# Kernel tuning notes

Measured on AMD Instinct MI355X. Metric: run time of the kernel, lower is better.

## Reference

```python
import jax, jax.numpy as jnp
import numpy as np

DIM = 1024
HEADS = 16
HEAD_DIM = DIM // HEADS
SCALE = DIM ** -0.5  # note: original uses full dim, not head_dim


def setup_inputs() -> dict:
    key = jax.random.key(0)
    k1, k2, k3, k4 = jax.random.split(key, 4)
    x = jax.random.normal(k1, (4, 2048, DIM), dtype=jnp.float32)
    # nn.Linear(dim, 3*dim, bias=False): weight [3*dim, dim]; y = x @ W.T
    w_qkv = jax.random.normal(k2, (3 * DIM, DIM), dtype=jnp.float32) * (DIM ** -0.5)
    w_out = jax.random.normal(k3, (DIM, DIM), dtype=jnp.float32) * (DIM ** -0.5)
    b_out = jax.random.normal(k4, (DIM,), dtype=jnp.float32) * 0.01
    return {"x": x, "w_qkv": w_qkv, "w_out": w_out, "b_out": b_out}


def reference(x, w_qkv, w_out, b_out):
    b, n, d = x.shape
    qkv = jnp.einsum('bnd,ed->bne', x, w_qkv)  # [b, n, 3*dim]
    # rearrange 'b n (qkv h d) -> qkv b h n d'
    qkv = qkv.reshape(b, n, 3, HEADS, HEAD_DIM).transpose(2, 0, 3, 1, 4)
    q, k, v = qkv[0], qkv[1], qkv[2]
    dots = jnp.einsum('bhid,bhjd->bhij', q, k) * SCALE
    attn = jax.nn.softmax(dots, axis=-1)
    out = jnp.einsum('bhij,bhjd->bhid', attn, v)
    out = out.transpose(0, 2, 1, 3).reshape(b, n, d)  # b h n d -> b n (h d)
    return jnp.einsum('bnd,ed->bne', out, w_out) + b_out
```

## Files before the change

kernel.cpp:

```cpp
#include <hip/hip_runtime.h>
#include <stdint.h>
#include <stddef.h>

typedef _Float16 f16;
typedef __attribute__((ext_vector_type(8))) _Float16 f16x8;
typedef __attribute__((ext_vector_type(4))) _Float16 f16x4;
typedef __attribute__((ext_vector_type(4))) float f32x4;

#define DINL __device__ __forceinline__

DINL void async_cp16(void* lds, const void* gmem) {
    __builtin_amdgcn_global_load_lds(
        (const __attribute__((address_space(1))) void*)(uintptr_t)gmem,
        (__attribute__((address_space(3))) void*)(uint32_t)(uintptr_t)lds,
        16, 0, 0);
}

__global__ void cast_fused(const float* __restrict__ x, f16* __restrict__ xh,
                           const float* __restrict__ wq, f16* __restrict__ wqh,
                           const float* __restrict__ wo, f16* __restrict__ woh,
                           float qs) {
    int stride = gridDim.x * blockDim.x;
    for (int i = blockIdx.x * blockDim.x + threadIdx.x; i < 3145728; i += stride) {
        const float4* src; f16x4* dst; float s = 1.f;
        if (i < 2097152)      { src = (const float4*)x  + i;            dst = (f16x4*)xh  + i; }
        else if (i < 2883584) { int j = i - 2097152; src = (const float4*)wq + j; dst = (f16x4*)wqh + j;
                                if (j < 262144) s = qs; }
        else                  { int j = i - 2883584; src = (const float4*)wo + j; dst = (f16x4*)woh + j; }
        float4 v = *src;
        f16x4 h = { (f16)(v.x * s), (f16)(v.y * s), (f16)(v.z * s), (f16)(v.w * s) };
        *dst = h;
    }
}

template <typename TC, bool HAS_BIAS>
__global__ __launch_bounds__(512, 2) void gemm8p(
    const f16* __restrict__ A, const f16* __restrict__ B,
    TC* __restrict__ C, const float* __restrict__ bias,
    int M, int N, int K)
{
    __shared__ __align__(16) char lds[98304];

    const int tid  = threadIdx.x;
    const int lane = tid & 63;
    const int wave = tid >> 6;
    const int rlo  = lane & 15;
    const int hi   = lane >> 4;
    const int wm   = wave & 3;
    const int wn   = wave >> 2;
    const int bm   = blockIdx.y * 256;
    const int bn   = blockIdx.x * 128;

    const int rA = tid >> 2;
    const int lc = (tid & 3) ^ ((tid >> 3) & 3);
    const f16* pA0 = A + (size_t)(bm + rA) * K + lc * 8;
    const f16* pA1 = A + (size_t)(bm + 128 + rA) * K + lc * 8;
    const f16* pB  = B + (size_t)(bn + rA) * K + lc * 8;
    const uint32_t dst0 = (uint32_t)tid * 16;
    const uint32_t dst1 = 8192u + (uint32_t)tid * 16;
    const uint32_t dstB = (uint32_t)tid * 16;

    const int fsw = (rlo >> 1) & 3;
    uint32_t afb[4], bfb[4];
#pragma unroll
    for (int m = 0; m < 4; ++m)
        afb[m] = (uint32_t)(wm * 64 + m * 16 + rlo) * 64 + (uint32_t)((hi ^ fsw) << 4);
#pragma unroll
    for (int n = 0; n < 4; ++n)
        bfb[n] = (uint32_t)(wn * 64 + n * 16 + rlo) * 64 + (uint32_t)((hi ^ fsw) << 4);

    f32x4 acc[4][4] = {};
    const int NP = K >> 5;

    auto stage = [&](int sg) {
        const uint32_t sa = (uint32_t)(sg & 3) << 14;
        const uint32_t sb = 65536u + ((uint32_t)(sg & 3) << 13);
        async_cp16(lds + sa + dst0, pA0);
        async_cp16(lds + sa + dst1, pA1);
        async_cp16(lds + sb + dstB, pB);
        pA0 += 32; pA1 += 32; pB += 32;
    };

    stage(0); stage(1); stage(2);

    for (int g = 0; g < NP; ++g) {
        if (g + 2 < NP)      asm volatile("s_waitcnt vmcnt(6)" ::: "memory");
        else if (g + 1 < NP) asm volatile("s_waitcnt vmcnt(3)" ::: "memory");
        else                 asm volatile("s_waitcnt vmcnt(0)" ::: "memory");
        __builtin_amdgcn_s_barrier();
        asm volatile("" ::: "memory");
        __builtin_amdgcn_sched_barrier(0);

        if (g + 3 < NP) stage(g + 3);

        const uint32_t sa = (uint32_t)(g & 3) << 14;
        const uint32_t sb = 65536u + ((uint32_t)(g & 3) << 13);

        f16x8 af[4], bf[4];
#pragma unroll
        for (int m = 0; m < 4; ++m)
            af[m] = *(const f16x8*)(lds + sa + afb[m]);
#pragma unroll
        for (int n = 0; n < 4; ++n)
            bf[n] = *(const f16x8*)(lds + sb + bfb[n]);

        __builtin_amdgcn_s_setprio(1);
#pragma unroll
        for (int m = 0; m < 4; ++m)
#pragma unroll
            for (int n = 0; n < 4; ++n)
                acc[m][n] = __builtin_amdgcn_mfma_f32_16x16x32_f16(af[m], bf[n], acc[m][n], 0, 0, 0);
        __builtin_amdgcn_s_setprio(0);
    }

#pragma unroll
    for (int n = 0; n < 4; ++n) {
        const int gc = bn + wn * 64 + n * 16 + rlo;
        float bv = 0.f;
        if constexpr (HAS_BIAS) bv = bias[gc];
#pragma unroll
        for (int m = 0; m < 4; ++m) {
            const int gr0 = bm + wm * 64 + m * 16 + (hi << 2);
#pragma unroll
            for (int r = 0; r < 4; ++r) {
                float v = acc[m][n][r] + bv;
                if constexpr (sizeof(TC) == 4) C[(size_t)(gr0 + r) * N + gc] = v;
                else                           C[(size_t)(gr0 + r) * N + gc] = (f16)v;
            }
        }
    }
}

__global__ __launch_bounds__(256) void transpose_v(const f16* __restrict__ qkv, f16* __restrict__ vt) {
    __shared__ float T[64][65];
    const int bid = blockIdx.x, bh = bid >> 5, st = bid & 31;
    const int b = bh >> 4, h = bh & 15, s0 = st * 64;
    const int tid = threadIdx.x;
    const int rs = tid >> 2, c0 = (tid & 3) * 16;
    const f16* src = &qkv[(size_t)(b * 2048 + s0 + rs) * 3072 + 2048 + h * 64 + c0];
    f16x8 v0 = ((const f16x8*)src)[0], v1 = ((const f16x8*)src)[1];
#pragma unroll
    for (int e = 0; e < 8; ++e) { T[rs][c0 + e] = (float)v0[e]; T[rs][c0 + 8 + e] = (float)v1[e]; }
    __syncthreads();
    const int rd = tid >> 2, k0 = (tid & 3) * 16;
    f16x8 w0, w1;
#pragma unroll
    for (int e = 0; e < 8; ++e) { w0[e] = (f16)T[k0 + e][rd]; w1[e] = (f16)T[k0 + 8 + e][rd]; }
    f16* dst = &vt[(size_t)(bh * 64 + rd) * 2048 + s0 + k0];
    ((f16x8*)dst)[0] = w0; ((f16x8*)dst)[1] = w1;
}

DINL int phi_row(int r) {
    return (r & 32) | ((r & 12) << 1) | ((r & 16) >> 2) | (r & 3);
}

__global__ __launch_bounds__(256, 4) void attn_mfma(
    const f16* __restrict__ qkv, const f16* __restrict__ vt, f16* __restrict__ out)
{
    constexpr int TD = 3072;
    constexpr int KSTR = 64 * TD;
    __shared__ __align__(16) f16 Ks[2][64 * 64];
    __shared__ __align__(16) f16 Vs[2][64 * 64];

    const int tid = threadIdx.x, lane = tid & 63, wave = tid >> 6;
    const int bh = blockIdx.x, b = bh >> 4, h = bh & 15;
    const int q0 = blockIdx.y * 128;
    const size_t base = (size_t)b * 2048 * TD + h * 64;
    const int lo = lane & 15, hi = lane >> 4;

    f16x8 qf[2][2];
#pragma unroll
    for (int g = 0; g < 2; ++g) {
        const f16* qp = &qkv[base + (size_t)(q0 + wave * 32 + g * 16 + lo) * TD + hi * 8];
        qf[g][0] = *(const f16x8*)qp;
        qf[g][1] = *(const f16x8*)(qp + 32);
    }

    const int s1 = tid,        r1 = s1 >> 3, c1 = (s1 & 7) ^ (r1 & 7);
    const int s2 = tid + 256,  r2 = s2 >> 3, c2 = (s2 & 7) ^ (r2 & 7);
    const f16* kg1 = &qkv[base + 1024 + (size_t)phi_row(r1) * TD + c1 * 8];
    const f16* kg2 = &qkv[base + 1024 + (size_t)phi_row(r2) * TD + c2 * 8];
    const f16* vg1 = &vt[(size_t)(bh * 64 + r1) * 2048 + c1 * 8];
    const f16* vg2 = &vt[(size_t)(bh * 64 + r2) * 2048 + c2 * 8];
    f16* kd1 = &Ks[0][s1 * 8]; f16* kd2 = &Ks[0][s2 * 8];
    f16* vd1 = &Vs[0][s1 * 8]; f16* vd2 = &Vs[0][s2 * 8];

    async_cp16(kd1, kg1); async_cp16(kd2, kg2);
    async_cp16(vd1, vg1); async_cp16(vd2, vg2);
    kg1 += KSTR; kg2 += KSTR; vg1 += 64; vg2 += 64;

    float lsum[2] = {};
    f32x4 o_[2][4] = {};

    for (int jt = 0; jt < 32; ++jt) {
        const int cur = jt & 1;
        __syncthreads();
        if (jt + 1 < 32) {
            const int nb = (cur ^ 1) * 4096;
            async_cp16(kd1 + nb, kg1); async_cp16(kd2 + nb, kg2);
            async_cp16(vd1 + nb, vg1); async_cp16(vd2 + nb, vg2);
            kg1 += KSTR; kg2 += KSTR; vg1 += 64; vg2 += 64;
        }

        f32x4 sc[2][4] = {{}, {}};
        __builtin_amdgcn_s_setprio(1);
#pragma unroll
        for (int ks = 0; ks < 2; ++ks) {
            const int c = ks * 4 + hi;
#pragma unroll
            for (int n = 0; n < 4; ++n) {
                int kr = n * 16 + lo;
                f16x8 kf = *(const f16x8*)&Ks[cur][(kr * 8 + (c ^ (kr & 7))) * 8];
                sc[0][n] = __builtin_amdgcn_mfma_f32_16x16x32_f16(kf, qf[0][ks], sc[0][n], 0, 0, 0);
                sc[1][n] = __builtin_amdgcn_mfma_f32_16x16x32_f16(kf, qf[1][ks], sc[1][n], 0, 0, 0);
            }
        }
        __builtin_amdgcn_s_setprio(0);

        f16x8 pa[2][2];
#pragma unroll
        for (int g = 0; g < 2; ++g)
#pragma unroll
        for (int n = 0; n < 4; ++n) {
            float p0 = exp2f(sc[g][n][0]), p1 = exp2f(sc[g][n][1]);
            float p2 = exp2f(sc[g][n][2]), p3 = exp2f(sc[g][n][3]);
            lsum[g] += (p0 + p1) + (p2 + p3);
            const int off = (n & 1) * 4;
            const int w = n >> 1;
            pa[g][w][off]   = (f16)p0; pa[g][w][off+1] = (f16)p1;
            pa[g][w][off+2] = (f16)p2; pa[g][w][off+3] = (f16)p3;
        }

        __builtin_amdgcn_s_setprio(1);
#pragma unroll
        for (int ks = 0; ks < 2; ++ks) {
            const int c = ks * 4 + hi;
#pragma unroll
            for (int n = 0; n < 4; ++n) {
                int dd = n * 16 + lo;
                f16x8 vb = *(const f16x8*)&Vs[cur][(dd * 8 + (c ^ (dd & 7))) * 8];
                o_[0][n] = __builtin_amdgcn_mfma_f32_16x16x32_f16(pa[0][ks], vb, o_[0][n], 0, 0, 0);
                o_[1][n] = __builtin_amdgcn_mfma_f32_16x16x32_f16(pa[1][ks], vb, o_[1][n], 0, 0, 0);
            }
        }
        __builtin_amdgcn_s_setprio(0);
    }

#pragma unroll
    for (int g = 0; g < 2; ++g) {
        float ls = lsum[g];
        ls += __shfl_xor(ls, 16);
        ls += __shfl_xor(ls, 32);
#pragma unroll
        for (int r = 0; r < 4; ++r) {
            float inv = 1.f / __shfl(ls, hi * 4 + r);
            int row = q0 + wave * 32 + g * 16 + hi * 4 + r;
#pragma unroll
            for (int n = 0; n < 4; ++n) {
                int dim = h * 64 + n * 16 + lo;
                out[(size_t)(b * 2048 + row) * 1024 + dim] = (f16)(o_[g][n][r] * inv);
            }
        }
    }
}

extern "C" void kernel_launch(void* const* d_in, const int* in_sizes, int n_in,
                              void* d_out, int out_size, void* d_ws, size_t ws_size,
                              hipStream_t stream)
{
    int ix = 0, iq = 1, iw = 2, ib = 3;
    for (int i = 0; i < n_in; ++i) {
        if      (in_sizes[i] == 8388608) ix = i;
        else if (in_sizes[i] == 3145728) iq = i;
        else if (in_sizes[i] == 1048576) iw = i;
        else if (in_sizes[i] == 1024)    ib = i;
    }
    const float* x     = (const float*)d_in[ix];
    const float* w_qkv = (const float*)d_in[iq];
    const float* w_out = (const float*)d_in[iw];
    const float* b_out = (const float*)d_in[ib];

    char* ws = (char*)d_ws;
    f16* Xh    = (f16*)(ws + 0);
    f16* AOh   = Xh;
    f16* Wqkvh = (f16*)(ws + 16777216);
    f16* QKVh  = (f16*)(ws + 23068672);
    f16* Vth   = (f16*)(ws + 73400320);
    f16* Wouth = (f16*)(ws + 90177536);

    const float QSCALE = 0.03125f * 1.4426950408889634f;

    cast_fused<<<3072, 256, 0, stream>>>(x, Xh, w_qkv, Wqkvh, w_out, Wouth, QSCALE);

    gemm8p<f16, false><<<dim3(24, 32), 512, 0, stream>>>(
        Xh, Wqkvh, QKVh, nullptr, 8192, 3072, 1024);

    transpose_v<<<2048, 256, 0, stream>>>(QKVh, Vth);

    attn_mfma<<<dim3(64, 16), 256, 0, stream>>>(QKVh, Vth, AOh);

    gemm8p<float, true><<<dim3(8, 32), 512, 0, stream>>>(
        AOh, Wouth, (float*)d_out, b_out, 8192, 1024, 1024);
}
```

Measured before the change: 290.1 us.

## Software-pipeline PV MFMA one tile behind QK with triple-buffered V

Restructures the attention loop so that the P·V matmul for the previous key tile runs after the current tile's QK^T MFMAs and before its exp2 softmax. The intent is to overlap exp/convert VALU work with MFMA work. V is now triple-buffered in LDS so the previous tile's V stays valid while the next one is being prefetched. Probabilities are also packed with cvt_pkrtz into f16 pairs instead of scalar casts. The cost is more LDS use per block, which may reduce occupancy, and higher register pressure from keeping pa live across iterations.

```diff
diff --git a/kernel.cpp b/kernel.cpp
--- a/kernel.cpp
+++ b/kernel.cpp
@@ -5,9 +5,14 @@
 typedef _Float16 f16;
 typedef __attribute__((ext_vector_type(8))) _Float16 f16x8;
 typedef __attribute__((ext_vector_type(4))) _Float16 f16x4;
+typedef __attribute__((ext_vector_type(2))) _Float16 f16x2;
 typedef __attribute__((ext_vector_type(4))) float f32x4;
 
 #define DINL __device__ __forceinline__
+
+DINL f16x2 pkrtz(float a, float b) {
+    return __builtin_bit_cast(f16x2, __builtin_amdgcn_cvt_pkrtz(a, b));
+}
 
 DINL void async_cp16(void* lds, const void* gmem) {
     __builtin_amdgcn_global_load_lds(
@@ -159,8 +164,8 @@
 {
     constexpr int TD = 3072;
     constexpr int KSTR = 64 * TD;
-    __shared__ __align__(16) f16 Ks[2][64 * 64];
-    __shared__ __align__(16) f16 Vs[2][64 * 64];
+    __shared__ __align__(16) f16 Ks[2][4096];
+    __shared__ __align__(16) f16 Vs[3][4096];
 
     const int tid = threadIdx.x, lane = tid & 63, wave = tid >> 6;
     const int bh = blockIdx.x, b = bh >> 4, h = bh & 15;
@@ -182,23 +187,24 @@
     const f16* kg2 = &qkv[base + 1024 + (size_t)phi_row(r2) * TD + c2 * 8];
     const f16* vg1 = &vt[(size_t)(bh * 64 + r1) * 2048 + c1 * 8];
     const f16* vg2 = &vt[(size_t)(bh * 64 + r2) * 2048 + c2 * 8];
-    f16* kd1 = &Ks[0][s1 * 8]; f16* kd2 = &Ks[0][s2 * 8];
-    f16* vd1 = &Vs[0][s1 * 8]; f16* vd2 = &Vs[0][s2 * 8];
-
-    async_cp16(kd1, kg1); async_cp16(kd2, kg2);
-    async_cp16(vd1, vg1); async_cp16(vd2, vg2);
+
+    async_cp16(&Ks[0][s1 * 8], kg1); async_cp16(&Ks[0][s2 * 8], kg2);
+    async_cp16(&Vs[0][s1 * 8], vg1); async_cp16(&Vs[0][s2 * 8], vg2);
     kg1 += KSTR; kg2 += KSTR; vg1 += 64; vg2 += 64;
 
     float lsum[2] = {};
     f32x4 o_[2][4] = {};
+    union PaU { f16x8 v8[2]; f16x2 h2[8]; };
+    PaU pa[2];
 
     for (int jt = 0; jt < 32; ++jt) {
-        const int cur = jt & 1;
+        const int kc = jt & 1;
         __syncthreads();
         if (jt + 1 < 32) {
-            const int nb = (cur ^ 1) * 4096;
-            async_cp16(kd1 + nb, kg1); async_cp16(kd2 + nb, kg2);
-            async_cp16(vd1 + nb, vg1); async_cp16(vd2 + nb, vg2);
+            const int kn = (jt + 1) & 1;
+            const int vn = (jt + 1) % 3;
+            async_cp16(&Ks[kn][s1 * 8], kg1); async_cp16(&Ks[kn][s2 * 8], kg2);
+            async_cp16(&Vs[vn][s1 * 8], vg1); async_cp16(&Vs[vn][s2 * 8], vg2);
             kg1 += KSTR; kg2 += KSTR; vg1 += 64; vg2 += 64;
         }
 
@@ -210,14 +216,30 @@
 #pragma unroll
             for (int n = 0; n < 4; ++n) {
                 int kr = n * 16 + lo;
-                f16x8 kf = *(const f16x8*)&Ks[cur][(kr * 8 + (c ^ (kr & 7))) * 8];
+                f16x8 kf = *(const f16x8*)&Ks[kc][(kr * 8 + (c ^ (kr & 7))) * 8];
                 sc[0][n] = __builtin_amdgcn_mfma_f32_16x16x32_f16(kf, qf[0][ks], sc[0][n], 0, 0, 0);
                 sc[1][n] = __builtin_amdgcn_mfma_f32_16x16x32_f16(kf, qf[1][ks], sc[1][n], 0, 0, 0);
             }
         }
         __builtin_amdgcn_s_setprio(0);
 
-        f16x8 pa[2][2];
+        if (jt) {
+            const int vp = (jt + 2) % 3;
+            __builtin_amdgcn_s_setprio(1);
+#pragma unroll
+            for (int ks = 0; ks < 2; ++ks) {
+                const int c = ks * 4 + hi;
+#pragma unroll
+                for (int n = 0; n < 4; ++n) {
+                    int dd = n * 16 + lo;
+                    f16x8 vb = *(const f16x8*)&Vs[vp][(dd * 8 + (c ^ (dd & 7))) * 8];
+                    o_[0][n] = __builtin_amdgcn_mfma_f32_16x16x32_f16(pa[0].v8[ks], vb, o_[0][n], 0, 0, 0);
+                    o_[1][n] = __builtin_amdgcn_mfma_f32_16x16x32_f16(pa[1].v8[ks], vb, o_[1][n], 0, 0, 0);
+                }
+            }
+            __builtin_amdgcn_s_setprio(0);
+        }
+
 #pragma unroll
         for (int g = 0; g < 2; ++g)
 #pragma unroll
@@ -225,25 +247,25 @@
             float p0 = exp2f(sc[g][n][0]), p1 = exp2f(sc[g][n][1]);
             float p2 = exp2f(sc[g][n][2]), p3 = exp2f(sc[g][n][3]);
             lsum[g] += (p0 + p1) + (p2 + p3);
-            const int off = (n & 1) * 4;
-            const int w = n >> 1;
-            pa[g][w][off]   = (f16)p0; pa[g][w][off+1] = (f16)p1;
-            pa[g][w][off+2] = (f16)p2; pa[g][w][off+3] = (f16)p3;
-        }
-
-        __builtin_amdgcn_s_setprio(1);
+            const int slot = (n >> 1) * 4 + (n & 1) * 2;
+            pa[g].h2[slot]     = pkrtz(p0, p1);
+            pa[g].h2[slot + 1] = pkrtz(p2, p3);
+        }
+    }
+
+    {
+        const int vp = 31 % 3;
 #pragma unroll
         for (int ks = 0; ks < 2; ++ks) {
             const int c = ks * 4 + hi;
 #pragma unroll
             for (int n = 0; n < 4; ++n) {
                 int dd = n * 16 + lo;
-                f16x8 vb = *(const f16x8*)&Vs[cur][(dd * 8 + (c ^ (dd & 7))) * 8];
-                o_[0][n] = __builtin_amdgcn_mfma_f32_16x16x32_f16(pa[0][ks], vb, o_[0][n], 0, 0, 0);
-                o_[1][n] = __builtin_amdgcn_mfma_f32_16x16x32_f16(pa[1][ks], vb, o_[1][n], 0, 0, 0);
-            }
-        }
-        __builtin_amdgcn_s_setprio(0);
+                f16x8 vb = *(const f16x8*)&Vs[vp][(dd * 8 + (c ^ (dd & 7))) * 8];
+                o_[0][n] = __builtin_amdgcn_mfma_f32_16x16x32_f16(pa[0].v8[ks], vb, o_[0][n], 0, 0, 0);
+                o_[1][n] = __builtin_amdgcn_mfma_f32_16x16x32_f16(pa[1].v8[ks], vb, o_[1][n], 0, 0, 0);
+            }
+        }
     }
 
 #pragma unroll
```

Result: slower. 309.3 us, median of 2 (+6.6%).
